# Performance work log

Hardware: AMD Instinct MI355X
Metric: run time of the kernel (lower is better)

Reference implementation:

```python
import jax, jax.numpy as jnp
import numpy as np
import math

D_MODEL = 1024
NUM_HEADS = 16
HEAD_DIM = D_MODEL // NUM_HEADS


def _sinusoidal_pe(seq_len, dim, dtype=jnp.float32):
    # Matches RotaryPositionEmbedding buffer: pe[:,0::2]=sin, pe[:,1::2]=cos
    pos = jnp.arange(seq_len, dtype=jnp.float32)[:, None]            # [S,1]
    div = jnp.exp(jnp.arange(0, dim, 2, dtype=jnp.float32) * (-math.log(10000.0) / dim))  # [dim/2]
    ang = pos * div[None, :]                                          # [S,dim/2]
    pe = jnp.stack([jnp.sin(ang), jnp.cos(ang)], axis=-1).reshape(seq_len, dim)
    return pe.astype(dtype)


def setup_inputs() -> dict:
    key = jax.random.key(0)
    ks = jax.random.split(key, 11)
    B, S, D = 4, 1024, D_MODEL
    s = 1.0 / math.sqrt(D)
    inp = {
        "q": jax.random.normal(ks[0], (B, S, D), jnp.float32),
        "k": jax.random.normal(ks[1], (B, S, D), jnp.float32),
        "v": jax.random.normal(ks[2], (B, S, D), jnp.float32),
        "Wq": jax.random.normal(ks[3], (D, D), jnp.float32) * s,
        "bq": jax.random.normal(ks[4], (D,), jnp.float32) * s,
        "Wk": jax.random.normal(ks[5], (D, D), jnp.float32) * s,
        "bk": jax.random.normal(ks[6], (D,), jnp.float32) * s,
        "Wv": jax.random.normal(ks[7], (D, D), jnp.float32) * s,
        "bv": jax.random.normal(ks[8], (D,), jnp.float32) * s,
        "Wo": jax.random.normal(ks[9], (D, D), jnp.float32) * s,
        "bo": jax.random.normal(ks[10], (D,), jnp.float32) * s,
    }
    return inp


def reference(q, k, v, Wq, bq, Wk, bk, Wv, bv, Wo, bo):
    B, S, D = q.shape
    H, hd = NUM_HEADS, HEAD_DIM
    scale = hd ** -0.5

    def proj(x, W, b):  # nn.Linear: x @ W.T + b, then [B,H,S,hd]
        return (x @ W.T + b).reshape(B, S, H, hd).transpose(0, 2, 1, 3)

    qh = proj(q, Wq, bq)
    kh = proj(k, Wk, bk)
    vh = proj(v, Wv, bv)

    pe = _sinusoidal_pe(S, hd, qh.dtype)[None, None]  # [1,1,S,hd]
    qh = qh + pe
    kh = kh + pe

    scores = jnp.einsum("bhqd,bhkd->bhqk", qh, kh) * scale  # [B,H,S,S]
    attn = jax.nn.softmax(scores, axis=-1)
    out = jnp.einsum("bhqk,bhkd->bhqd", attn, vh)            # [B,H,S,hd]
    out = out.transpose(0, 2, 1, 3).reshape(B, S, D)
    return out @ Wo.T + bo
```

## Files before the change

### kernel.cpp

```cpp
#include <hip/hip_runtime.h>
#include <hip/hip_bf16.h>

#define B_  4
#define S_  1024
#define D_  1024
#define H_  16
#define HD_ 64

typedef __bf16 bf16;
typedef __bf16 bf16x8 __attribute__((ext_vector_type(8)));
typedef __bf16 bf16x4 __attribute__((ext_vector_type(4)));
typedef float  f32x4  __attribute__((ext_vector_type(4)));

__device__ __forceinline__ void gll16(const void* g, void* l) {
    __builtin_amdgcn_global_load_lds((__attribute__((address_space(1))) void*)(void*)g,
                                     (__attribute__((address_space(3))) void*)l,
                                     16, 0, 0);
}

__global__ __launch_bounds__(256)
void convert_all_kernel(const float* __restrict__ q, const float* __restrict__ k,
                        const float* __restrict__ v,
                        const float* __restrict__ Wq, const float* __restrict__ Wk,
                        const float* __restrict__ Wv, const float* __restrict__ Wo,
                        bf16* __restrict__ Xb, bf16* __restrict__ Wall)
{
    const size_t e = ((size_t)blockIdx.x * 256 + threadIdx.x) * 8;
    const size_t M4 = (size_t)1 << 22;
    const float* s;
    bf16* d;
    if (e < 3 * M4) {
        const int which = (int)(e >> 22);
        s = ((which == 0) ? q : (which == 1) ? k : v) + (e - ((size_t)which << 22));
        d = Xb + e;
    } else {
        const size_t r = e - 3 * M4;
        const int which = (int)(r >> 20);
        s = ((which == 0) ? Wq : (which == 1) ? Wk : (which == 2) ? Wv : Wo) +
            (r - ((size_t)which << 20));
        d = Wall + r;
    }
    const f32x4 a = *(const f32x4*)s;
    const f32x4 b = *(const f32x4*)(s + 4);
    bf16x8 o;
#pragma unroll
    for (int jj = 0; jj < 4; ++jj) { o[jj] = (bf16)a[jj]; o[jj + 4] = (bf16)b[jj]; }
    *(bf16x8*)d = o;
}

__global__ __launch_bounds__(256)
void convert_w_kernel(const float* __restrict__ Wq, const float* __restrict__ Wk,
                      const float* __restrict__ Wv, const float* __restrict__ Wo,
                      bf16* __restrict__ dst)
{
    const int idx   = blockIdx.x * 256 + threadIdx.x;
    const int which = idx >> 17;
    const int off   = (idx & 131071) * 8;
    const float* s  = (which == 0) ? Wq : (which == 1) ? Wk : (which == 2) ? Wv : Wo;
    const f32x4 a = *(const f32x4*)(s + off);
    const f32x4 b = *(const f32x4*)(s + off + 4);
    bf16x8 o;
#pragma unroll
    for (int jj = 0; jj < 4; ++jj) { o[jj] = (bf16)a[jj]; o[jj + 4] = (bf16)b[jj]; }
    *(bf16x8*)(dst + ((size_t)which << 20) + off) = o;
}

__device__ __forceinline__ void qkv_epilogue(
    f32x4 (&acc)[4][4], int z, int m0, int n0, int mw, int nw, int lr, int lg,
    const float* __restrict__ bias,
    bf16* __restrict__ Qh, bf16* __restrict__ Kh, bf16* __restrict__ Vt)
{
    if (z < 2) {
        bf16* dst = (z == 0) ? Qh : Kh;
        const float sc = (z == 0) ? 0.125f : 1.0f;
#pragma unroll
        for (int i = 0; i < 4; ++i) {
#pragma unroll
            for (int j = 0; j < 4; ++j) {
                const int n = n0 + nw + 16 * j + lr;
                const int h = n >> 6, d = n & 63;
                const float bn = bias[n];
                const float dv_rev = 0.15915494309189535f *
                    exp2f(-(float)(d & ~1) * 0.20762050593046648f);
#pragma unroll
                for (int r = 0; r < 4; ++r) {
                    const int m = m0 + mw + 16 * i + lg * 4 + r;
                    const int b = m >> 10, s = m & 1023;
                    float rev = (float)s * dv_rev;
                    rev -= floorf(rev);
                    const float sv = __builtin_amdgcn_sinf(rev);
                    const float cv = __builtin_amdgcn_cosf(rev);
                    const float pe  = (d & 1) ? cv : sv;
                    const float val = (acc[i][j][r] + bn + pe) * sc;
                    dst[(size_t)((b * H_ + h) * S_ + s) * HD_ + d] = (bf16)val;
                }
            }
        }
    } else {
#pragma unroll
        for (int i = 0; i < 4; ++i) {
            const int mb = m0 + mw + 16 * i + lg * 4;
            const int b = mb >> 10, sb = mb & 1023;
#pragma unroll
            for (int j = 0; j < 4; ++j) {
                const int n = n0 + nw + 16 * j + lr;
                const int h = n >> 6, d = n & 63;
                const float bn = bias[n];
                bf16x4 pk;
#pragma unroll
                for (int r = 0; r < 4; ++r) pk[r] = (bf16)(acc[i][j][r] + bn);
                *(bf16x4*)(Vt + (size_t)((b * H_ + h) * HD_ + d) * S_ + sb) = pk;
            }
        }
    }
}

__global__ __launch_bounds__(256)
void qkv_proj_bf16_kernel(const bf16* __restrict__ Xb, const bf16* __restrict__ Wall,
                          const float* __restrict__ bq, const float* __restrict__ bk,
                          const float* __restrict__ bv,
                          bf16* __restrict__ Qh, bf16* __restrict__ Kh,
                          bf16* __restrict__ Vt)
{
    __shared__ __align__(16) bf16 sA[128 * 32];
    __shared__ __align__(16) bf16 sB[128 * 32];

    const int blk  = blockIdx.x;
    const int mIdx = blk & 31;
    const int t    = blk >> 5;
    const int nIdx = t & 7;
    const int z    = t >> 3;

    const int m0 = mIdx * 128, n0 = nIdx * 128;
    const bf16* __restrict__ X = Xb + ((size_t)z << 22);
    const bf16* __restrict__ W = Wall + ((size_t)z << 20);
    const float* __restrict__ bias = (z == 0) ? bq : (z == 1) ? bk : bv;

    const int tid  = threadIdx.x;
    const int lane = tid & 63;
    const int wave = tid >> 6;
    const int lr   = lane & 15;
    const int lg   = lane >> 4;
    const int mw   = (wave >> 1) * 64;
    const int nw   = (wave & 1) * 64;
    const int srow = tid >> 2;
    const int skg  = (tid & 3) * 8;

    f32x4 acc[4][4];
#pragma unroll
    for (int i = 0; i < 4; ++i)
#pragma unroll
        for (int j = 0; j < 4; ++j) acc[i][j] = (f32x4){0.f, 0.f, 0.f, 0.f};

    const bf16* Ab = X + (size_t)(m0 + srow) * D_ + skg;
    const bf16* Wb = W + (size_t)(n0 + srow) * D_ + skg;

    for (int kt = 0; kt < 32; ++kt) {
        const int k0 = kt * 32;
        __syncthreads();
#pragma unroll
        for (int p = 0; p < 2; ++p) {
            gll16(Ab + (size_t)(p * 64) * D_ + k0, (char*)sA + p * 4096 + tid * 16);
            gll16(Wb + (size_t)(p * 64) * D_ + k0, (char*)sB + p * 4096 + tid * 16);
        }
        __syncthreads();

        bf16x8 af[4], bfr[4];
#pragma unroll
        for (int i = 0; i < 4; ++i)
            af[i] = *(const bf16x8*)(sA + (mw + 16 * i + lr) * 32 + lg * 8);
#pragma unroll
        for (int j = 0; j < 4; ++j)
            bfr[j] = *(const bf16x8*)(sB + (nw + 16 * j + lr) * 32 + lg * 8);
#pragma unroll
        for (int i = 0; i < 4; ++i)
#pragma unroll
            for (int j = 0; j < 4; ++j)
                acc[i][j] = __builtin_amdgcn_mfma_f32_16x16x32_bf16(af[i], bfr[j],
                                                                    acc[i][j], 0, 0, 0);
    }
    qkv_epilogue(acc, z, m0, n0, mw, nw, lr, lg, bias, Qh, Kh, Vt);
}

__global__ __launch_bounds__(256)
void qkv_proj_mixed_kernel(const float* __restrict__ qin, const float* __restrict__ kin,
                           const float* __restrict__ vin,
                           const bf16* __restrict__ Wall,
                           const float* __restrict__ bq, const float* __restrict__ bk,
                           const float* __restrict__ bv,
                           bf16* __restrict__ Qh, bf16* __restrict__ Kh,
                           bf16* __restrict__ Vt)
{
    __shared__ __align__(16) bf16 sA[128 * 32];
    __shared__ __align__(16) bf16 sB[128 * 32];

    const int z = blockIdx.z;
    const float* __restrict__ X    = (z == 0) ? qin : (z == 1) ? kin : vin;
    const float* __restrict__ bias = (z == 0) ? bq  : (z == 1) ? bk  : bv;

    const int m0   = blockIdx.y * 128;
    const int n0   = blockIdx.x * 128;
    const int tid  = threadIdx.x;
    const int lane = tid & 63;
    const int wave = tid >> 6;
    const int lr   = lane & 15;
    const int lg   = lane >> 4;
    const int mw   = (wave >> 1) * 64;
    const int nw   = (wave & 1) * 64;
    const int srow = tid >> 2;
    const int skg  = (tid & 3) * 8;

    f32x4 acc[4][4];
#pragma unroll
    for (int i = 0; i < 4; ++i)
#pragma unroll
        for (int j = 0; j < 4; ++j) acc[i][j] = (f32x4){0.f, 0.f, 0.f, 0.f};

    const float* Ab = X + (size_t)(m0 + srow) * D_ + skg;
    const bf16*  Wb = Wall + ((size_t)z << 20) + (size_t)(n0 + srow) * D_ + skg;

    for (int kt = 0; kt < 32; ++kt) {
        const int k0 = kt * 32;
        f32x4 ga[2][2];
#pragma unroll
        for (int p = 0; p < 2; ++p) {
            const float* ar = Ab + (size_t)(p * 64) * D_ + k0;
            ga[p][0] = *(const f32x4*)(ar);
            ga[p][1] = *(const f32x4*)(ar + 4);
        }
        __syncthreads();
#pragma unroll
        for (int p = 0; p < 2; ++p)
            gll16(Wb + (size_t)(p * 64) * D_ + k0, (char*)sB + p * 4096 + tid * 16);
#pragma unroll
        for (int p = 0; p < 2; ++p) {
            bf16x8 ta;
#pragma unroll
            for (int jj = 0; jj < 4; ++jj) {
                ta[jj]     = (bf16)ga[p][0][jj];
                ta[jj + 4] = (bf16)ga[p][1][jj];
            }
            *(bf16x8*)(sA + p * 2048 + tid * 8) = ta;
        }
        __syncthreads();

        bf16x8 af[4], bfr[4];
#pragma unroll
        for (int i = 0; i < 4; ++i)
            af[i] = *(const bf16x8*)(sA + (mw + 16 * i + lr) * 32 + lg * 8);
#pragma unroll
        for (int j = 0; j < 4; ++j)
            bfr[j] = *(const bf16x8*)(sB + (nw + 16 * j + lr) * 32 + lg * 8);
#pragma unroll
        for (int i = 0; i < 4; ++i)
#pragma unroll
            for (int j = 0; j < 4; ++j)
                acc[i][j] = __builtin_amdgcn_mfma_f32_16x16x32_bf16(af[i], bfr[j],
                                                                    acc[i][j], 0, 0, 0);
    }
    qkv_epilogue(acc, z, m0, n0, mw, nw, lr, lg, bias, Qh, Kh, Vt);
}

#define LDK 72
__global__ __launch_bounds__(256)
void attn_kernel(const bf16* __restrict__ Qh, const bf16* __restrict__ Kh,
                 const bf16* __restrict__ Vt, bf16* __restrict__ att)
{
    __shared__ __align__(16) bf16 sK[64 * LDK];
    __shared__ __align__(16) bf16 sV[64 * LDK];
    __shared__ __align__(16) bf16 sP[4 * 32 * LDK];

    const int tid  = threadIdx.x;
    const int lane = tid & 63;
    const int wave = tid >> 6;
    const int lr   = lane & 15;
    const int lg   = lane >> 4;
    const int bh   = blockIdx.x & 63;
    const int qt   = blockIdx.x >> 6;
    const int qw   = qt * 128 + wave * 32;

    const bf16* Qb = Qh + (size_t)bh * S_ * HD_;
    const bf16* Kb = Kh + (size_t)bh * S_ * HD_;
    const bf16* Vb = Vt + (size_t)bh * HD_ * S_;

    bf16x8 qa[2][2];
#pragma unroll
    for (int i = 0; i < 2; ++i)
#pragma unroll
        for (int ks = 0; ks < 2; ++ks)
            qa[i][ks] = *(const bf16x8*)(Qb + (size_t)(qw + 16 * i + lr) * HD_ +
                                         ks * 32 + lg * 8);

    f32x4 o[2][4];
    float lsum[2][4];
#pragma unroll
    for (int i = 0; i < 2; ++i) {
#pragma unroll
        for (int jd = 0; jd < 4; ++jd) o[i][jd] = (f32x4){0.f, 0.f, 0.f, 0.f};
#pragma unroll
        for (int r = 0; r < 4; ++r) lsum[i][r] = 0.f;
    }

    bf16* const pw   = sP + wave * 32 * LDK;
    const int  srow  = tid >> 3;
    const int  scol  = (tid & 7) * 8;

    bf16x8 kv[2], vv[2];
#pragma unroll
    for (int p = 0; p < 2; ++p) {
        kv[p] = *(const bf16x8*)(Kb + (size_t)(p * 32 + srow) * HD_ + scol);
        vv[p] = *(const bf16x8*)(Vb + (size_t)(p * 32 + srow) * S_ + scol);
    }

    for (int kc = 0; kc < 16; ++kc) {
        __syncthreads();
#pragma unroll
        for (int p = 0; p < 2; ++p) {
            *(bf16x8*)(sK + (p * 32 + srow) * LDK + scol) = kv[p];
            *(bf16x8*)(sV + (p * 32 + srow) * LDK + scol) = vv[p];
        }
        __syncthreads();

        if (kc < 15) {
            const int kn = (kc + 1) * 64;
#pragma unroll
            for (int p = 0; p < 2; ++p) {
                kv[p] = *(const bf16x8*)(Kb + (size_t)(kn + p * 32 + srow) * HD_ + scol);
                vv[p] = *(const bf16x8*)(Vb + (size_t)(p * 32 + srow) * S_ + kn + scol);
            }
        }

        bf16x8 kb[4][2];
#pragma unroll
        for (int jk = 0; jk < 4; ++jk)
#pragma unroll
            for (int ks = 0; ks < 2; ++ks)
                kb[jk][ks] = *(const bf16x8*)(sK + (16 * jk + lr) * LDK + ks * 32 + lg * 8);

#pragma unroll
        for (int i = 0; i < 2; ++i)
#pragma unroll
            for (int jk = 0; jk < 4; ++jk) {
                f32x4 s = (f32x4){0.f, 0.f, 0.f, 0.f};
                s = __builtin_amdgcn_mfma_f32_16x16x32_bf16(qa[i][0], kb[jk][0], s, 0, 0, 0);
                s = __builtin_amdgcn_mfma_f32_16x16x32_bf16(qa[i][1], kb[jk][1], s, 0, 0, 0);
#pragma unroll
                for (int r = 0; r < 4; ++r) {
                    const float pp = __expf(s[r]);
                    lsum[i][r] += pp;
                    pw[(16 * i + lg * 4 + r) * LDK + 16 * jk + lr] = (bf16)pp;
                }
            }
        asm volatile("s_waitcnt lgkmcnt(0)" ::: "memory");

#pragma unroll
        for (int ks = 0; ks < 2; ++ks) {
            bf16x8 pa[2];
#pragma unroll
            for (int i = 0; i < 2; ++i)
                pa[i] = *(const bf16x8*)(pw + (16 * i + lr) * LDK + ks * 32 + lg * 8);
#pragma unroll
            for (int jd = 0; jd < 4; ++jd) {
                const bf16x8 vb = *(const bf16x8*)(sV + (16 * jd + lr) * LDK +
                                                   ks * 32 + lg * 8);
#pragma unroll
                for (int i = 0; i < 2; ++i)
                    o[i][jd] = __builtin_amdgcn_mfma_f32_16x16x32_bf16(pa[i], vb,
                                                                       o[i][jd], 0, 0, 0);
            }
        }
    }

    const int b = bh >> 4, h = bh & 15;
#pragma unroll
    for (int i = 0; i < 2; ++i)
#pragma unroll
        for (int r = 0; r < 4; ++r) {
            float l = lsum[i][r];
#pragma unroll
            for (int off = 1; off < 16; off <<= 1)
                l += __shfl_xor(l, off, 64);
            const float inv = 1.f / l;
            const int s = qw + 16 * i + lg * 4 + r;
#pragma unroll
            for (int jd = 0; jd < 4; ++jd) {
                const int d = 16 * jd + lr;
                att[(size_t)(b * S_ + s) * D_ + h * HD_ + d] = (bf16)(o[i][jd][r] * inv);
            }
        }
}

__global__ __launch_bounds__(256)
void out_proj_kernel(const bf16* __restrict__ A, const bf16* __restrict__ Wob,
                     const float* __restrict__ bo, float* __restrict__ out)
{
    __shared__ __align__(16) bf16 sA[64 * 32];
    __shared__ __align__(16) bf16 sB[128 * 32];

    const int blk  = blockIdx.x;
    const int mIdx = blk & 63;
    const int nIdx = blk >> 6;
    const int m0 = mIdx * 64, n0 = nIdx * 128;

    const int tid  = threadIdx.x;
    const int lane = tid & 63;
    const int wave = tid >> 6;
    const int lr   = lane & 15;
    const int lg   = lane >> 4;
    const int mw   = (wave >> 1) * 32;
    const int nw   = (wave & 1) * 64;
    const int srow = tid >> 2;
    const int skg  = (tid & 3) * 8;

    f32x4 acc[2][4];
#pragma unroll
    for (int i = 0; i < 2; ++i)
#pragma unroll
        for (int j = 0; j < 4; ++j) acc[i][j] = (f32x4){0.f, 0.f, 0.f, 0.f};

    const bf16* Ab = A   + (size_t)(m0 + srow) * D_ + skg;
    const bf16* Wb = Wob + (size_t)(n0 + srow) * D_ + skg;

    for (int kt = 0; kt < 32; ++kt) {
        const int k0 = kt * 32;
        __syncthreads();
        gll16(Ab + k0, (char*)sA + tid * 16);
#pragma unroll
        for (int p = 0; p < 2; ++p)
            gll16(Wb + (size_t)(p * 64) * D_ + k0, (char*)sB + p * 4096 + tid * 16);
        __syncthreads();

        bf16x8 af[2], bfr[4];
#pragma unroll
        for (int i = 0; i < 2; ++i)
            af[i] = *(const bf16x8*)(sA + (mw + 16 * i + lr) * 32 + lg * 8);
#pragma unroll
        for (int j = 0; j < 4; ++j)
            bfr[j] = *(const bf16x8*)(sB + (nw + 16 * j + lr) * 32 + lg * 8);
#pragma unroll
        for (int i = 0; i < 2; ++i)
#pragma unroll
            for (int j = 0; j < 4; ++j)
                acc[i][j] = __builtin_amdgcn_mfma_f32_16x16x32_bf16(af[i], bfr[j],
                                                                    acc[i][j], 0, 0, 0);
    }

#pragma unroll
    for (int i = 0; i < 2; ++i)
#pragma unroll
        for (int j = 0; j < 4; ++j) {
            const int n = n0 + nw + 16 * j + lr;
            const float bn = bo[n];
#pragma unroll
            for (int r = 0; r < 4; ++r) {
                const int m = m0 + mw + 16 * i + lg * 4 + r;
                out[(size_t)m * D_ + n] = acc[i][j][r] + bn;
            }
        }
}

extern "C" void kernel_launch(void* const* d_in, const int* in_sizes, int n_in,
                              void* d_out, int out_size, void* d_ws, size_t ws_size,
                              hipStream_t stream)
{
    const float* q  = (const float*)d_in[0];
    const float* k  = (const float*)d_in[1];
    const float* v  = (const float*)d_in[2];
    const float* Wq = (const float*)d_in[3];
    const float* bq = (const float*)d_in[4];
    const float* Wk = (const float*)d_in[5];
    const float* bk = (const float*)d_in[6];
    const float* Wv = (const float*)d_in[7];
    const float* bv = (const float*)d_in[8];
    const float* Wo = (const float*)d_in[9];
    const float* bo = (const float*)d_in[10];

    char* ws = (char*)d_ws;
    const size_t MB8 = (size_t)8 * 1024 * 1024;
    bf16* Qh  = (bf16*)(ws);
    bf16* Kh  = (bf16*)(ws + MB8);
    bf16* Vt  = (bf16*)(ws + 2 * MB8);
    bf16* att = (bf16*)(ws + 3 * MB8);

    if (ws_size >= (size_t)64 * 1024 * 1024) {
        bf16* Xb   = (bf16*)(ws + 4 * MB8);
        bf16* Wall = (bf16*)(ws + 7 * MB8);
        convert_all_kernel<<<8192, 256, 0, stream>>>(q, k, v, Wq, Wk, Wv, Wo,
                                                     Xb, Wall);
        qkv_proj_bf16_kernel<<<768, 256, 0, stream>>>(Xb, Wall, bq, bk, bv,
                                                      Qh, Kh, Vt);
        attn_kernel<<<512, 256, 0, stream>>>(Qh, Kh, Vt, att);
        out_proj_kernel<<<512, 256, 0, stream>>>(att, Wall + ((size_t)3 << 20),
                                                 bo, (float*)d_out);
    } else {
        bf16* Wall = (bf16*)d_out;
        convert_w_kernel<<<2048, 256, 0, stream>>>(Wq, Wk, Wv, Wo, Wall);
        qkv_proj_mixed_kernel<<<dim3(8, 32, 3), 256, 0, stream>>>(
            q, k, v, Wall, bq, bk, bv, Qh, Kh, Vt);
        attn_kernel<<<512, 256, 0, stream>>>(Qh, Kh, Vt, att);
        hipMemcpyAsync((void*)Qh, (const void*)(Wall + ((size_t)3 << 20)),
                       (size_t)D_ * D_ * sizeof(bf16), hipMemcpyDeviceToDevice,
                       stream);
        out_proj_kernel<<<512, 256, 0, stream>>>(att, (const bf16*)Qh, bo,
                                                 (float*)d_out);
    }
}
```

Baseline: 217.0 us.

## Double-buffer shared memory tiles in projection GEMMs and attention loop

Doubles the LDS staging buffers in the QKV projection, out-projection and attention kernels so the next K-tile is fetched into one buffer while the current one is consumed. This removes one __syncthreads per iteration and lets global-to-LDS loads overlap the MFMA work. In exchange it raises LDS use per block, which may lower occupancy, especially in the attention kernel.

```diff
diff --git a/kernel.cpp b/kernel.cpp
--- a/kernel.cpp
+++ b/kernel.cpp
@@ -122,8 +122,8 @@
                           bf16* __restrict__ Qh, bf16* __restrict__ Kh,
                           bf16* __restrict__ Vt)
 {
-    __shared__ __align__(16) bf16 sA[128 * 32];
-    __shared__ __align__(16) bf16 sB[128 * 32];
+    __shared__ __align__(16) bf16 sA[2 * 128 * 32];
+    __shared__ __align__(16) bf16 sB[2 * 128 * 32];
 
     const int blk  = blockIdx.x;
     const int mIdx = blk & 31;
@@ -155,23 +155,35 @@
     const bf16* Ab = X + (size_t)(m0 + srow) * D_ + skg;
     const bf16* Wb = W + (size_t)(n0 + srow) * D_ + skg;
 
+#pragma unroll
+    for (int p = 0; p < 2; ++p) {
+        gll16(Ab + (size_t)(p * 64) * D_, (char*)sA + p * 4096 + tid * 16);
+        gll16(Wb + (size_t)(p * 64) * D_, (char*)sB + p * 4096 + tid * 16);
+    }
+
     for (int kt = 0; kt < 32; ++kt) {
-        const int k0 = kt * 32;
+        const int cur = kt & 1, nxt = cur ^ 1;
         __syncthreads();
-#pragma unroll
-        for (int p = 0; p < 2; ++p) {
-            gll16(Ab + (size_t)(p * 64) * D_ + k0, (char*)sA + p * 4096 + tid * 16);
-            gll16(Wb + (size_t)(p * 64) * D_ + k0, (char*)sB + p * 4096 + tid * 16);
-        }
-        __syncthreads();
-
+        if (kt < 31) {
+            const int k1 = (kt + 1) * 32;
+#pragma unroll
+            for (int p = 0; p < 2; ++p) {
+                gll16(Ab + (size_t)(p * 64) * D_ + k1,
+                      (char*)sA + nxt * 8192 + p * 4096 + tid * 16);
+                gll16(Wb + (size_t)(p * 64) * D_ + k1,
+                      (char*)sB + nxt * 8192 + p * 4096 + tid * 16);
+            }
+        }
+
+        const bf16* a = sA + cur * 4096;
+        const bf16* b = sB + cur * 4096;
         bf16x8 af[4], bfr[4];
 #pragma unroll
         for (int i = 0; i < 4; ++i)
-            af[i] = *(const bf16x8*)(sA + (mw + 16 * i + lr) * 32 + lg * 8);
+            af[i] = *(const bf16x8*)(a + (mw + 16 * i + lr) * 32 + lg * 8);
 #pragma unroll
         for (int j = 0; j < 4; ++j)
-            bfr[j] = *(const bf16x8*)(sB + (nw + 16 * j + lr) * 32 + lg * 8);
+            bfr[j] = *(const bf16x8*)(b + (nw + 16 * j + lr) * 32 + lg * 8);
 #pragma unroll
         for (int i = 0; i < 4; ++i)
 #pragma unroll
@@ -266,8 +278,8 @@
 void attn_kernel(const bf16* __restrict__ Qh, const bf16* __restrict__ Kh,
                  const bf16* __restrict__ Vt, bf16* __restrict__ att)
 {
-    __shared__ __align__(16) bf16 sK[64 * LDK];
-    __shared__ __align__(16) bf16 sV[64 * LDK];
+    __shared__ __align__(16) bf16 sK[2 * 64 * LDK];
+    __shared__ __align__(16) bf16 sV[2 * 64 * LDK];
     __shared__ __align__(16) bf16 sP[4 * 32 * LDK];
 
     const int tid  = threadIdx.x;
@@ -313,11 +325,13 @@
     }
 
     for (int kc = 0; kc < 16; ++kc) {
-        __syncthreads();
+        const int cur = kc & 1;
+        bf16* const sKc = sK + cur * 64 * LDK;
+        bf16* const sVc = sV + cur * 64 * LDK;
 #pragma unroll
         for (int p = 0; p < 2; ++p) {
-            *(bf16x8*)(sK + (p * 32 + srow) * LDK + scol) = kv[p];
-            *(bf16x8*)(sV + (p * 32 + srow) * LDK + scol) = vv[p];
+            *(bf16x8*)(sKc + (p * 32 + srow) * LDK + scol) = kv[p];
+            *(bf16x8*)(sVc + (p * 32 + srow) * LDK + scol) = vv[p];
         }
         __syncthreads();
 
@@ -335,7 +349,7 @@
         for (int jk = 0; jk < 4; ++jk)
 #pragma unroll
             for (int ks = 0; ks < 2; ++ks)
-                kb[jk][ks] = *(const bf16x8*)(sK + (16 * jk + lr) * LDK + ks * 32 + lg * 8);
+                kb[jk][ks] = *(const bf16x8*)(sKc + (16 * jk + lr) * LDK + ks * 32 + lg * 8);
 
 #pragma unroll
         for (int i = 0; i < 2; ++i)
@@ -361,7 +375,7 @@
                 pa[i] = *(const bf16x8*)(pw + (16 * i + lr) * LDK + ks * 32 + lg * 8);
 #pragma unroll
             for (int jd = 0; jd < 4; ++jd) {
-                const bf16x8 vb = *(const bf16x8*)(sV + (16 * jd + lr) * LDK +
+                const bf16x8 vb = *(const bf16x8*)(sVc + (16 * jd + lr) * LDK +
                                                    ks * 32 + lg * 8);
 #pragma unroll
                 for (int i = 0; i < 2; ++i)
@@ -394,8 +408,8 @@
 void out_proj_kernel(const bf16* __restrict__ A, const bf16* __restrict__ Wob,
                      const float* __restrict__ bo, float* __restrict__ out)
 {
-    __shared__ __align__(16) bf16 sA[64 * 32];
-    __shared__ __align__(16) bf16 sB[128 * 32];
+    __shared__ __align__(16) bf16 sA[2 * 64 * 32];
+    __shared__ __align__(16) bf16 sB[2 * 128 * 32];
 
     const int blk  = blockIdx.x;
     const int mIdx = blk & 63;
@@ -421,22 +435,32 @@
     const bf16* Ab = A   + (size_t)(m0 + srow) * D_ + skg;
     const bf16* Wb = Wob + (size_t)(n0 + srow) * D_ + skg;
 
+    gll16(Ab, (char*)sA + tid * 16);
+#pragma unroll
+    for (int p = 0; p < 2; ++p)
+        gll16(Wb + (size_t)(p * 64) * D_, (char*)sB + p * 4096 + tid * 16);
+
     for (int kt = 0; kt < 32; ++kt) {
-        const int k0 = kt * 32;
+        const int cur = kt & 1, nxt = cur ^ 1;
         __syncthreads();
-        gll16(Ab + k0, (char*)sA + tid * 16);
-#pragma unroll
-        for (int p = 0; p < 2; ++p)
-            gll16(Wb + (size_t)(p * 64) * D_ + k0, (char*)sB + p * 4096 + tid * 16);
-        __syncthreads();
-
+        if (kt < 31) {
+            const int k1 = (kt + 1) * 32;
+            gll16(Ab + k1, (char*)sA + nxt * 4096 + tid * 16);
+#pragma unroll
+            for (int p = 0; p < 2; ++p)
+                gll16(Wb + (size_t)(p * 64) * D_ + k1,
+                      (char*)sB + nxt * 8192 + p * 4096 + tid * 16);
+        }
+
+        const bf16* a = sA + cur * 2048;
+        const bf16* b = sB + cur * 4096;
         bf16x8 af[2], bfr[4];
 #pragma unroll
         for (int i = 0; i < 2; ++i)
-            af[i] = *(const bf16x8*)(sA + (mw + 16 * i + lr) * 32 + lg * 8);
+            af[i] = *(const bf16x8*)(a + (mw + 16 * i + lr) * 32 + lg * 8);
 #pragma unroll
         for (int j = 0; j < 4; ++j)
-            bfr[j] = *(const bf16x8*)(sB + (nw + 16 * j + lr) * 32 + lg * 8);
+            bfr[j] = *(const bf16x8*)(b + (nw + 16 * j + lr) * 32 + lg * 8);
 #pragma unroll
         for (int i = 0; i < 2; ++i)
 #pragma unroll
```

After: 225.9 us. +4.1%, slower.
